# Kernel tuning notes

Measured on AMD Instinct MI355X. Metric: run time of the kernel, lower is better.

Reference implementation:

```python
import jax, jax.numpy as jnp
import numpy as np

N = 100_000      # nodes
E = 1_600_000    # edges (avg degree 16)
F_IN = 128       # in_feats
H = 128          # n_hidden
H2 = 64          # n_hidden // 2


def setup_inputs() -> dict:
    key = jax.random.key(0)
    k1, k2, k3, k4, k5 = jax.random.split(key, 5)
    features = jax.random.normal(k1, (N, F_IN), dtype=jnp.float32)
    W1 = jax.random.normal(k2, (F_IN, H), dtype=jnp.float32) * 0.05
    W2 = jax.random.normal(k3, (H, H2), dtype=jnp.float32) * 0.05
    src = jax.random.randint(k4, (E,), 0, N, dtype=jnp.int32)
    dst = jax.random.randint(k5, (E,), 0, N, dtype=jnp.int32)
    return {"features": features, "W1": W1, "W2": W2, "src": src, "dst": dst}


def _graph_conv(h, W, src, dst, out_norm, in_norm):
    # DGL GraphConv, norm='both', bias=False:
    #   rst = D_dst^{-1/2} * (A @ (D_src^{-1/2} * h)) @ W
    # (weight applied before/after aggregation is mathematically identical)
    h = h * out_norm[:, None]                                   # scale source feats
    agg = jax.ops.segment_sum(h[src], dst, num_segments=N)      # SpMM: sum over in-edges
    return (agg * in_norm[:, None]) @ W


def reference(features, W1, W2, src, dst):
    ones = jnp.ones(src.shape[0], dtype=jnp.float32)
    # allow_zero_in_degree=True -> DGL clamps degrees to min 1 for norm
    out_deg = jnp.clip(jax.ops.segment_sum(ones, src, num_segments=N), 1.0)
    in_deg = jnp.clip(jax.ops.segment_sum(ones, dst, num_segments=N), 1.0)
    out_norm = out_deg ** -0.5
    in_norm = in_deg ** -0.5
    h = _graph_conv(features, W1, src, dst, out_norm, in_norm)  # [N, H]
    h = jax.nn.relu(h)
    return _graph_conv(h, W2, src, dst, out_norm, in_norm)      # [N, H2]
```

## Files before the change

kernel.cpp:

```cpp
#include <hip/hip_runtime.h>
#include <cstdint>
#include <cstddef>

#define NN 100000
#define NE 1600000
#define FD 128
#define HD2 64

#define BSH 7
#define BSZ 128
#define NB ((NN + BSZ - 1) / BSZ)
#define TILE 4096
#define NTILE ((NE + TILE - 1) / TILE)
#define CAPB 2560
#define NPREP ((NN * 32 + FD * 64 + HD2 * 64 + 255) / 256)

static_assert(NB <= 1024, "bucket scan assumes <=1024 buckets");

typedef short bf16x8_t __attribute__((ext_vector_type(8)));
typedef float f32x4_t __attribute__((ext_vector_type(4)));
typedef unsigned char uchar;

static __device__ __forceinline__ uint f2bf(float x) {
  uint u = __float_as_uint(x);
  return (u + 0x7fffu + ((u >> 16) & 1u)) >> 16;
}
static __device__ __forceinline__ uint pack2(float lo, float hi) {
  return f2bf(lo) | (f2bf(hi) << 16);
}
static __device__ __forceinline__ float bflo(uint v) { return __uint_as_float(v << 16); }
static __device__ __forceinline__ float bfhi(uint v) { return __uint_as_float(v & 0xffff0000u); }

static __device__ __forceinline__ float dec_w(uint r) {
  return __uint_as_float(((r >> 17) + 0x38000u) << 12);
}

__global__ void k_bucket_prep(const int* __restrict__ src, const int* __restrict__ dst,
                              int* __restrict__ bcnt_d, int* __restrict__ bcnt_s,
                              uint* __restrict__ brec_d, uchar* __restrict__ brec_s,
                              const float* __restrict__ feat, uint* __restrict__ Xraw,
                              const float* __restrict__ W1, const float* __restrict__ W2,
                              uint* __restrict__ W1t, uint* __restrict__ W2t) {
  __shared__ int h[NB];
  __shared__ int gb[NB];
  __shared__ int ls[NB];
  __shared__ int psum[256];
  __shared__ int ntot;
  __shared__ ushort bkt[TILE];
  __shared__ uint lrec[TILE];
  const int bid = blockIdx.x;
  const int t = threadIdx.x;
  if (bid >= 2 * NTILE) {
    int i = (bid - 2 * NTILE) * 256 + t;
    if (i < NN * 32) {
      float4 f = *(const float4*)(feat + 4 * (size_t)i);
      uint2 o;
      o.x = pack2(f.x, f.y);
      o.y = pack2(f.z, f.w);
      *(uint2*)(Xraw + 2 * (size_t)i) = o;
    } else {
      int j = i - NN * 32;
      if (j < FD * 64) {
        int n = j >> 6, kk = j & 63;
        W1t[j] = pack2(W1[(size_t)(2 * kk) * FD + n], W1[(size_t)(2 * kk + 1) * FD + n]);
      } else if (j < FD * 64 + HD2 * 64) {
        int j2 = j - FD * 64;
        int n = j2 >> 6, kk = j2 & 63;
        W2t[j2] = pack2(W2[(size_t)(2 * kk) * HD2 + n], W2[(size_t)(2 * kk + 1) * HD2 + n]);
      }
    }
    return;
  }
  const bool is_dst = bid < NTILE;
  const int* key = is_dst ? dst : src;
  const int base = (is_dst ? bid : bid - NTILE) * TILE;
  for (int i = t; i < NB; i += 256) h[i] = 0;
  __syncthreads();
  for (int i = t; i < TILE; i += 256) {
    int e = base + i;
    if (e < NE) atomicAdd(&h[key[e] >> BSH], 1);
  }
  __syncthreads();
  int* bcnt = is_dst ? bcnt_d : bcnt_s;
  for (int i = t; i < NB; i += 256) {
    int c = h[i];
    gb[i] = c ? atomicAdd(bcnt + i, c) : 0;
  }
  int i0 = t * 4;
  int c0 = (i0 + 0 < NB) ? h[i0 + 0] : 0;
  int c1 = (i0 + 1 < NB) ? h[i0 + 1] : 0;
  int c2 = (i0 + 2 < NB) ? h[i0 + 2] : 0;
  int c3 = (i0 + 3 < NB) ? h[i0 + 3] : 0;
  int cs = c0 + c1 + c2 + c3;
  psum[t] = cs;
  __syncthreads();
#pragma unroll
  for (int off = 1; off < 256; off <<= 1) {
    int x = (t >= off) ? psum[t - off] : 0;
    __syncthreads();
    psum[t] += x;
    __syncthreads();
  }
  int excl = psum[t] - cs;
  if (i0 + 0 < NB) ls[i0 + 0] = excl;
  if (i0 + 1 < NB) ls[i0 + 1] = excl + c0;
  if (i0 + 2 < NB) ls[i0 + 2] = excl + c0 + c1;
  if (i0 + 3 < NB) ls[i0 + 3] = excl + c0 + c1 + c2;
  if (t == 255) ntot = psum[255];
  __syncthreads();
  for (int i = t; i < NB; i += 256) h[i] = 0;
  __syncthreads();
  if (is_dst) {
    for (int i = t; i < TILE; i += 256) {
      int e = base + i;
      if (e < NE) {
        int d = dst[e], sv = src[e];
        int b = d >> BSH;
        int q = ls[b] + atomicAdd(&h[b], 1);
        lrec[q] = ((uint)(d & (BSZ - 1)) << 17) | (uint)sv;
        bkt[q] = (ushort)b;
      }
    }
  } else {
    for (int i = t; i < TILE; i += 256) {
      int e = base + i;
      if (e < NE) {
        int sv = src[e];
        int b = sv >> BSH;
        int q = ls[b] + atomicAdd(&h[b], 1);
        lrec[q] = (uint)(sv & (BSZ - 1));
        bkt[q] = (ushort)b;
      }
    }
  }
  __syncthreads();
  const int n = ntot;
  if (is_dst) {
    for (int q = t; q < n; q += 256) {
      int b = bkt[q];
      int p = gb[b] + (q - ls[b]);
      if (p < CAPB) brec_d[(size_t)b * CAPB + p] = lrec[q];
    }
  } else {
    for (int q = t; q < n; q += 256) {
      int b = bkt[q];
      int p = gb[b] + (q - ls[b]);
      if (p < CAPB) brec_s[(size_t)b * CAPB + p] = (uchar)lrec[q];
    }
  }
}

__global__ __launch_bounds__(1024) void k_onorm_scan(const uchar* __restrict__ brec_s,
                                                     const int* __restrict__ bcnt_s,
                                                     float* __restrict__ out_norm,
                                                     const int* __restrict__ bcnt_d,
                                                     int* __restrict__ boff_d) {
  __shared__ int sm[1024];
  const int t = threadIdx.x;
  const int b = blockIdx.x;
  if (b < NB) {
    if (t < BSZ) sm[t] = 0;
    __syncthreads();
    const int len = min(bcnt_s[b], CAPB);
    const size_t rbase = (size_t)b * CAPB;
    for (int e = t; e < len; e += 1024)
      atomicAdd(&sm[brec_s[rbase + e]], 1);
    __syncthreads();
    const int s0 = b * BSZ;
    const int ns = min(BSZ, NN - s0);
    if (t < ns) out_norm[s0 + t] = rsqrtf((float)max(sm[t], 1));
  } else {
    int v = (t < NB) ? bcnt_d[t] : 0;
    sm[t] = v;
    __syncthreads();
#pragma unroll
    for (int off = 1; off < 1024; off <<= 1) {
      int x = (t >= off) ? sm[t - off] : 0;
      __syncthreads();
      sm[t] += x;
      __syncthreads();
    }
    if (t < NB) boff_d[t + 1] = sm[t];
    if (t == 0) boff_d[0] = 0;
  }
}

__global__ __launch_bounds__(256) void k_build(const uint* __restrict__ brec_d,
                                               const int* __restrict__ bcnt_d,
                                               const int* __restrict__ boff,
                                               const float* __restrict__ onorm,
                                               int* __restrict__ row_ptr,
                                               float* __restrict__ in_norm,
                                               uint* __restrict__ csr) {
  __shared__ int lcnt[BSZ];
  __shared__ int lscan[BSZ + 1];
  __shared__ int lcur[BSZ];
  __shared__ int lcsr[CAPB];
  const int t = threadIdx.x;
  const int b = blockIdx.x;
  const int d0 = b * BSZ;
  const int nd = min(BSZ, NN - d0);
  const size_t rbase = (size_t)b * CAPB;
  const int len = min(bcnt_d[b], CAPB);
  const int ebase = boff[b];

  for (int i = t; i < BSZ; i += 256) lcnt[i] = 0;
  __syncthreads();
  for (int e = t; e < len; e += 256)
    atomicAdd(&lcnt[brec_d[rbase + e] >> 17], 1);
  __syncthreads();
  for (int i = t; i < nd; i += 256)
    in_norm[d0 + i] = rsqrtf((float)max(lcnt[i], 1));

  if (t < BSZ) lcur[t] = lcnt[t];
  __syncthreads();
#pragma unroll
  for (int off = 1; off < BSZ; off <<= 1) {
    int x = (t >= off && t < BSZ) ? lcur[t - off] : 0;
    __syncthreads();
    if (t < BSZ) lcur[t] += x;
    __syncthreads();
  }
  if (t < BSZ) lscan[t + 1] = lcur[t];
  if (t == 0) lscan[0] = 0;
  __syncthreads();
  for (int i = t; i <= nd; i += 256) row_ptr[d0 + i] = ebase + lscan[i];
  if (t < BSZ) lcur[t] = lscan[t];
  __syncthreads();

  for (int e = t; e < len; e += 256) {
    uint r = brec_d[rbase + e];
    int p = atomicAdd(&lcur[r >> 17], 1);
    lcsr[p] = (int)(r & 0x1FFFFu);
  }
  __syncthreads();
  for (int ld = t; ld < nd; ld += 256) {
    int a = lscan[ld], bnd = lscan[ld + 1];
    for (int i = a + 1; i < bnd; ++i) {
      int v = lcsr[i];
      int j = i - 1;
      while (j >= a && lcsr[j] > v) { lcsr[j + 1] = lcsr[j]; --j; }
      lcsr[j + 1] = v;
    }
  }
  __syncthreads();
  for (int i = t; i < len; i += 256) {
    int s = lcsr[i];
    uint code = (__float_as_uint(onorm[s]) >> 12) - 0x38000u;
    csr[ebase + i] = (code << 17) | (uint)s;
  }
}

__global__ void k_spmm1b(const uint* __restrict__ Xraw, const int* __restrict__ row_ptr,
                         const uint* __restrict__ csr, const float* __restrict__ in_norm,
                         uint* __restrict__ Hb1) {
  int gid = blockIdx.x * blockDim.x + threadIdx.x;
  int row = gid >> 6;
  if (row >= NN) return;
  int lane = threadIdx.x & 63;
  int grp = lane >> 4;
  int gl = lane & 15;
  int e0 = row_ptr[row], e1 = row_ptr[row + 1];
  float2 a0 = {0.f, 0.f}, a1 = {0.f, 0.f}, a2 = {0.f, 0.f}, a3 = {0.f, 0.f};
#define ACCW(v, ww)                                                       \
  a0.x = fmaf(ww, bflo((v).x), a0.x); a0.y = fmaf(ww, bfhi((v).x), a0.y); \
  a1.x = fmaf(ww, bflo((v).y), a1.x); a1.y = fmaf(ww, bfhi((v).y), a1.y); \
  a2.x = fmaf(ww, bflo((v).z), a2.x); a2.y = fmaf(ww, bfhi((v).z), a2.y); \
  a3.x = fmaf(ww, bflo((v).w), a3.x); a3.y = fmaf(ww, bfhi((v).w), a3.y);
  int e = e0;
  for (; e + 16 <= e1; e += 16) {
    uint r0 = csr[e + grp];
    uint r1 = csr[e + 4 + grp];
    uint r2 = csr[e + 8 + grp];
    uint r3 = csr[e + 12 + grp];
    uint4 v0 = *(const uint4*)(Xraw + ((size_t)(r0 & 0x1FFFFu) << 6) + (gl << 2));
    uint4 v1 = *(const uint4*)(Xraw + ((size_t)(r1 & 0x1FFFFu) << 6) + (gl << 2));
    uint4 v2 = *(const uint4*)(Xraw + ((size_t)(r2 & 0x1FFFFu) << 6) + (gl << 2));
    uint4 v3 = *(const uint4*)(Xraw + ((size_t)(r3 & 0x1FFFFu) << 6) + (gl << 2));
    float w0 = dec_w(r0), w1 = dec_w(r1), w2 = dec_w(r2), w3 = dec_w(r3);
    ACCW(v0, w0);
    ACCW(v1, w1);
    ACCW(v2, w2);
    ACCW(v3, w3);
  }
  for (; e + 4 <= e1; e += 4) {
    uint r0 = csr[e + grp];
    uint4 v0 = *(const uint4*)(Xraw + ((size_t)(r0 & 0x1FFFFu) << 6) + (gl << 2));
    float w0 = dec_w(r0);
    ACCW(v0, w0);
  }
  if (e + grp < e1) {
    uint r0 = csr[e + grp];
    uint4 v0 = *(const uint4*)(Xraw + ((size_t)(r0 & 0x1FFFFu) << 6) + (gl << 2));
    float w0 = dec_w(r0);
    ACCW(v0, w0);
  }
#undef ACCW
#pragma unroll
  for (int m = 16; m <= 32; m <<= 1) {
    a0.x += __shfl_xor(a0.x, m); a0.y += __shfl_xor(a0.y, m);
    a1.x += __shfl_xor(a1.x, m); a1.y += __shfl_xor(a1.y, m);
    a2.x += __shfl_xor(a2.x, m); a2.y += __shfl_xor(a2.y, m);
    a3.x += __shfl_xor(a3.x, m); a3.y += __shfl_xor(a3.y, m);
  }
  if (grp == 0) {
    float wi = in_norm[row];
    uint4 o;
    o.x = pack2(a0.x * wi, a0.y * wi);
    o.y = pack2(a1.x * wi, a1.y * wi);
    o.z = pack2(a2.x * wi, a2.y * wi);
    o.w = pack2(a3.x * wi, a3.y * wi);
    *(uint4*)(Hb1 + ((size_t)row << 6) + (gl << 2)) = o;
  }
}

__global__ __launch_bounds__(256) void k_mlp(const uint* __restrict__ Hb1,
                                             const uint* __restrict__ W1t,
                                             const uint* __restrict__ W2t,
                                             const float* __restrict__ onorm,
                                             ushort* __restrict__ Tb) {
  __shared__ ushort h_lds[64 * FD];
  char* const lds = (char*)h_lds;
  const int tid = threadIdx.x;
  const int wid = tid >> 6;
  const int lane = tid & 63;
  const int l15 = lane & 15;
  const int g = lane >> 4;
  const int rowbase = blockIdx.x * 64 + wid * 16;

  const int ar = min(rowbase + l15, NN - 1);
  const uint* Arow = Hb1 + (size_t)ar * 64;
  bf16x8_t afr[4];
#pragma unroll
  for (int kc = 0; kc < 4; ++kc)
    afr[kc] = *(const bf16x8_t*)(Arow + kc * 16 + g * 4);

  float wnorm[4];
#pragma unroll
  for (int r = 0; r < 4; ++r)
    wnorm[r] = onorm[min(rowbase + 4 * g + r, NN - 1)];

#pragma unroll
  for (int nf = 0; nf < 8; ++nf) {
    f32x4_t acc = {0.f, 0.f, 0.f, 0.f};
#pragma unroll
    for (int kc = 0; kc < 4; ++kc) {
      bf16x8_t b = *(const bf16x8_t*)(W1t + (size_t)(nf * 16 + l15) * 64 + kc * 16 + g * 4);
      acc = __builtin_amdgcn_mfma_f32_16x16x32_bf16(afr[kc], b, acc, 0, 0, 0);
    }
#pragma unroll
    for (int r = 0; r < 4; ++r) {
      float hv = fmaxf(acc[r], 0.f) * wnorm[r];
      int row = wid * 16 + 4 * g + r;
      int byte = row * 256 + (nf * 16 + l15) * 2;
      byte ^= (row & 7) << 4;
      *(ushort*)(lds + byte) = (ushort)f2bf(hv);
    }
  }
  __syncthreads();

  bf16x8_t a2[4];
#pragma unroll
  for (int kc = 0; kc < 4; ++kc) {
    int row = wid * 16 + l15;
    int byte = row * 256 + (kc * 32 + 8 * g) * 2;
    byte ^= (row & 7) << 4;
    a2[kc] = *(const bf16x8_t*)(lds + byte);
  }
#pragma unroll
  for (int nf = 0; nf < 4; ++nf) {
    f32x4_t acc = {0.f, 0.f, 0.f, 0.f};
#pragma unroll
    for (int kc = 0; kc < 4; ++kc) {
      bf16x8_t b = *(const bf16x8_t*)(W2t + (size_t)(nf * 16 + l15) * 64 + kc * 16 + g * 4);
      acc = __builtin_amdgcn_mfma_f32_16x16x32_bf16(a2[kc], b, acc, 0, 0, 0);
    }
#pragma unroll
    for (int r = 0; r < 4; ++r) {
      int row = rowbase + 4 * g + r;
      if (row < NN)
        Tb[(size_t)row * HD2 + nf * 16 + l15] = (ushort)f2bf(acc[r]);
    }
  }
}

__global__ void k_spmm2b(const uint* __restrict__ Tb, const int* __restrict__ row_ptr,
                         const uint* __restrict__ csr, const float* __restrict__ in_norm,
                         float* __restrict__ out) {
  int gid = blockIdx.x * blockDim.x + threadIdx.x;
  int row = gid >> 6;
  if (row >= NN) return;
  int lane = threadIdx.x & 63;
  int grp = lane >> 4;
  int gl = lane & 15;
  int e0 = row_ptr[row], e1 = row_ptr[row + 1];
  float2 a0 = {0.f, 0.f}, a1 = {0.f, 0.f};
#define ACC2(v)                                  \
  a0.x += bflo((v).x); a0.y += bfhi((v).x);      \
  a1.x += bflo((v).y); a1.y += bfhi((v).y);
  int e = e0;
  for (; e + 16 <= e1; e += 16) {
    uint s0 = csr[e + grp] & 0x1FFFFu;
    uint s1 = csr[e + 4 + grp] & 0x1FFFFu;
    uint s2 = csr[e + 8 + grp] & 0x1FFFFu;
    uint s3 = csr[e + 12 + grp] & 0x1FFFFu;
    uint2 v0 = *(const uint2*)(Tb + ((size_t)s0 << 5) + (gl << 1));
    uint2 v1 = *(const uint2*)(Tb + ((size_t)s1 << 5) + (gl << 1));
    uint2 v2 = *(const uint2*)(Tb + ((size_t)s2 << 5) + (gl << 1));
    uint2 v3 = *(const uint2*)(Tb + ((size_t)s3 << 5) + (gl << 1));
    ACC2(v0);
    ACC2(v1);
    ACC2(v2);
    ACC2(v3);
  }
  for (; e + 4 <= e1; e += 4) {
    uint s0 = csr[e + grp] & 0x1FFFFu;
    uint2 v0 = *(const uint2*)(Tb + ((size_t)s0 << 5) + (gl << 1));
    ACC2(v0);
  }
  if (e + grp < e1) {
    uint s0 = csr[e + grp] & 0x1FFFFu;
    uint2 v0 = *(const uint2*)(Tb + ((size_t)s0 << 5) + (gl << 1));
    ACC2(v0);
  }
#undef ACC2
#pragma unroll
  for (int m = 16; m <= 32; m <<= 1) {
    a0.x += __shfl_xor(a0.x, m); a0.y += __shfl_xor(a0.y, m);
    a1.x += __shfl_xor(a1.x, m); a1.y += __shfl_xor(a1.y, m);
  }
  if (grp == 0) {
    float wi = in_norm[row];
    *(float4*)(out + (size_t)row * HD2 + gl * 4) =
        make_float4(a0.x * wi, a0.y * wi, a1.x * wi, a1.y * wi);
  }
}

extern "C" void kernel_launch(void* const* d_in, const int* in_sizes, int n_in,
                              void* d_out, int out_size, void* d_ws, size_t ws_size,
                              hipStream_t stream) {
  const float* feat = (const float*)d_in[0];
  const float* W1   = (const float*)d_in[1];
  const float* W2   = (const float*)d_in[2];
  const int*   src  = (const int*)d_in[3];
  const int*   dst  = (const int*)d_in[4];
  float* out = (float*)d_out;

  char* p = (char*)d_ws;
  auto take = [&p](size_t bytes) -> char* {
    char* r = p;
    p += (bytes + 511) & ~(size_t)511;
    return r;
  };
  int*   row_ptr  = (int*)take((size_t)(NN + 1) * 4);
  int*   bcnt     = (int*)take((size_t)2 * NB * 4);
  int*   boff_d   = (int*)take((size_t)(NB + 1) * 4);
  float* out_norm = (float*)take((size_t)NN * 4);
  float* in_norm  = (float*)take((size_t)NN * 4);
  uint*  csr      = (uint*)take((size_t)NE * 4);
  uint*  W1t      = (uint*)take((size_t)FD * 64 * 4);
  uint*  W2t      = (uint*)take((size_t)HD2 * 64 * 4);
  uint*  Xraw     = (uint*)take((size_t)NN * 64 * 4);
  uint*  Hb1      = (uint*)take((size_t)NN * 64 * 4);
  int*   bcnt_d   = bcnt;
  int*   bcnt_s   = bcnt + NB;
  ushort* Tb      = (ushort*)Xraw;
  uint*   brec_d  = (uint*)Hb1;
  uchar*  brec_s  = (uchar*)(Hb1 + (size_t)NB * CAPB);

  hipMemsetAsync(bcnt, 0, (size_t)2 * NB * 4, stream);

  k_bucket_prep<<<2 * NTILE + NPREP, 256, 0, stream>>>(src, dst, bcnt_d, bcnt_s, brec_d, brec_s,
                                                       feat, Xraw, W1, W2, W1t, W2t);
  k_onorm_scan <<<NB + 1, 1024, 0, stream>>>(brec_s, bcnt_s, out_norm, bcnt_d, boff_d);
  k_build      <<<NB, 256, 0, stream>>>(brec_d, bcnt_d, boff_d, out_norm,
                                        row_ptr, in_norm, csr);

  k_spmm1b<<<(NN * 64) / 256, 256, 0, stream>>>(Xraw, row_ptr, csr, in_norm, Hb1);
  k_mlp   <<<(NN + 63) / 64, 256, 0, stream>>>(Hb1, W1t, W2t, out_norm, Tb);
  k_spmm2b<<<(NN * 64) / 256, 256, 0, stream>>>((const uint*)Tb, row_ptr, csr, in_norm, out);
}
```

Before: 256.2 us.

## Split SpMM feature columns across two blocks per row group

```diff
diff --git a/kernel.cpp b/kernel.cpp
--- a/kernel.cpp
+++ b/kernel.cpp
@@ -16,6 +16,7 @@
 #define NPREP ((NN * 32 + FD * 64 + HD2 * 64 + 255) / 256)
 
 static_assert(NB <= 1024, "bucket scan assumes <=1024 buckets");
+static_assert(NN % 16 == 0, "spmm row mapping assumes NN % 16 == 0");
 
 typedef short bf16x8_t __attribute__((ext_vector_type(8)));
 typedef float f32x4_t __attribute__((ext_vector_type(4)));
@@ -254,29 +255,30 @@
 __global__ void k_spmm1b(const uint* __restrict__ Xraw, const int* __restrict__ row_ptr,
                          const uint* __restrict__ csr, const float* __restrict__ in_norm,
                          uint* __restrict__ Hb1) {
-  int gid = blockIdx.x * blockDim.x + threadIdx.x;
-  int row = gid >> 6;
+  const int bid = blockIdx.x;
+  const int g8 = bid >> 3, r8 = bid & 7;
+  const int cg = r8 >> 2;
+  const int row = (g8 * 4 + (r8 & 3)) * 4 + (threadIdx.x >> 6);
   if (row >= NN) return;
-  int lane = threadIdx.x & 63;
-  int grp = lane >> 4;
-  int gl = lane & 15;
+  const int lane = threadIdx.x & 63;
+  const int grp = lane >> 4;
+  const int gl = lane & 15;
+  const uint coff = (uint)(cg * 32 + gl * 2);
   int e0 = row_ptr[row], e1 = row_ptr[row + 1];
-  float2 a0 = {0.f, 0.f}, a1 = {0.f, 0.f}, a2 = {0.f, 0.f}, a3 = {0.f, 0.f};
+  float2 a0 = {0.f, 0.f}, a1 = {0.f, 0.f};
 #define ACCW(v, ww)                                                       \
   a0.x = fmaf(ww, bflo((v).x), a0.x); a0.y = fmaf(ww, bfhi((v).x), a0.y); \
-  a1.x = fmaf(ww, bflo((v).y), a1.x); a1.y = fmaf(ww, bfhi((v).y), a1.y); \
-  a2.x = fmaf(ww, bflo((v).z), a2.x); a2.y = fmaf(ww, bfhi((v).z), a2.y); \
-  a3.x = fmaf(ww, bflo((v).w), a3.x); a3.y = fmaf(ww, bfhi((v).w), a3.y);
+  a1.x = fmaf(ww, bflo((v).y), a1.x); a1.y = fmaf(ww, bfhi((v).y), a1.y);
   int e = e0;
   for (; e + 16 <= e1; e += 16) {
     uint r0 = csr[e + grp];
     uint r1 = csr[e + 4 + grp];
     uint r2 = csr[e + 8 + grp];
     uint r3 = csr[e + 12 + grp];
-    uint4 v0 = *(const uint4*)(Xraw + ((size_t)(r0 & 0x1FFFFu) << 6) + (gl << 2));
-    uint4 v1 = *(const uint4*)(Xraw + ((size_t)(r1 & 0x1FFFFu) << 6) + (gl << 2));
-    uint4 v2 = *(const uint4*)(Xraw + ((size_t)(r2 & 0x1FFFFu) << 6) + (gl << 2));
-    uint4 v3 = *(const uint4*)(Xraw + ((size_t)(r3 & 0x1FFFFu) << 6) + (gl << 2));
+    uint2 v0 = *(const uint2*)(Xraw + ((size_t)(r0 & 0x1FFFFu) << 6) + coff);
+    uint2 v1 = *(const uint2*)(Xraw + ((size_t)(r1 & 0x1FFFFu) << 6) + coff);
+    uint2 v2 = *(const uint2*)(Xraw + ((size_t)(r2 & 0x1FFFFu) << 6) + coff);
+    uint2 v3 = *(const uint2*)(Xraw + ((size_t)(r3 & 0x1FFFFu) << 6) + coff);
     float w0 = dec_w(r0), w1 = dec_w(r1), w2 = dec_w(r2), w3 = dec_w(r3);
     ACCW(v0, w0);
     ACCW(v1, w1);
@@ -285,13 +287,13 @@
   }
   for (; e + 4 <= e1; e += 4) {
     uint r0 = csr[e + grp];
-    uint4 v0 = *(const uint4*)(Xraw + ((size_t)(r0 & 0x1FFFFu) << 6) + (gl << 2));
+    uint2 v0 = *(const uint2*)(Xraw + ((size_t)(r0 & 0x1FFFFu) << 6) + coff);
     float w0 = dec_w(r0);
     ACCW(v0, w0);
   }
   if (e + grp < e1) {
     uint r0 = csr[e + grp];
-    uint4 v0 = *(const uint4*)(Xraw + ((size_t)(r0 & 0x1FFFFu) << 6) + (gl << 2));
+    uint2 v0 = *(const uint2*)(Xraw + ((size_t)(r0 & 0x1FFFFu) << 6) + coff);
     float w0 = dec_w(r0);
     ACCW(v0, w0);
   }
@@ -300,17 +302,13 @@
   for (int m = 16; m <= 32; m <<= 1) {
     a0.x += __shfl_xor(a0.x, m); a0.y += __shfl_xor(a0.y, m);
     a1.x += __shfl_xor(a1.x, m); a1.y += __shfl_xor(a1.y, m);
-    a2.x += __shfl_xor(a2.x, m); a2.y += __shfl_xor(a2.y, m);
-    a3.x += __shfl_xor(a3.x, m); a3.y += __shfl_xor(a3.y, m);
   }
   if (grp == 0) {
     float wi = in_norm[row];
-    uint4 o;
+    uint2 o;
     o.x = pack2(a0.x * wi, a0.y * wi);
     o.y = pack2(a1.x * wi, a1.y * wi);
-    o.z = pack2(a2.x * wi, a2.y * wi);
-    o.w = pack2(a3.x * wi, a3.y * wi);
-    *(uint4*)(Hb1 + ((size_t)row << 6) + (gl << 2)) = o;
+    *(uint2*)(Hb1 + ((size_t)row << 6) + coff) = o;
   }
 }
 
@@ -387,27 +385,28 @@
 __global__ void k_spmm2b(const uint* __restrict__ Tb, const int* __restrict__ row_ptr,
                          const uint* __restrict__ csr, const float* __restrict__ in_norm,
                          float* __restrict__ out) {
-  int gid = blockIdx.x * blockDim.x + threadIdx.x;
-  int row = gid >> 6;
+  const int bid = blockIdx.x;
+  const int g8 = bid >> 3, r8 = bid & 7;
+  const int cg = r8 >> 2;
+  const int row = (g8 * 4 + (r8 & 3)) * 4 + (threadIdx.x >> 6);
   if (row >= NN) return;
-  int lane = threadIdx.x & 63;
-  int grp = lane >> 4;
-  int gl = lane & 15;
+  const int lane = threadIdx.x & 63;
+  const int grp = lane >> 4;
+  const int gl = lane & 15;
+  const uint coff = (uint)(cg * 16 + gl);
   int e0 = row_ptr[row], e1 = row_ptr[row + 1];
-  float2 a0 = {0.f, 0.f}, a1 = {0.f, 0.f};
-#define ACC2(v)                                  \
-  a0.x += bflo((v).x); a0.y += bfhi((v).x);      \
-  a1.x += bflo((v).y); a1.y += bfhi((v).y);
+  float2 a0 = {0.f, 0.f};
+#define ACC2(v)  a0.x += bflo(v); a0.y += bfhi(v);
   int e = e0;
   for (; e + 16 <= e1; e += 16) {
     uint s0 = csr[e + grp] & 0x1FFFFu;
     uint s1 = csr[e + 4 + grp] & 0x1FFFFu;
     uint s2 = csr[e + 8 + grp] & 0x1FFFFu;
     uint s3 = csr[e + 12 + grp] & 0x1FFFFu;
-    uint2 v0 = *(const uint2*)(Tb + ((size_t)s0 << 5) + (gl << 1));
-    uint2 v1 = *(const uint2*)(Tb + ((size_t)s1 << 5) + (gl << 1));
-    uint2 v2 = *(const uint2*)(Tb + ((size_t)s2 << 5) + (gl << 1));
-    uint2 v3 = *(const uint2*)(Tb + ((size_t)s3 << 5) + (gl << 1));
+    uint v0 = Tb[((size_t)s0 << 5) + coff];
+    uint v1 = Tb[((size_t)s1 << 5) + coff];
+    uint v2 = Tb[((size_t)s2 << 5) + coff];
+    uint v3 = Tb[((size_t)s3 << 5) + coff];
     ACC2(v0);
     ACC2(v1);
     ACC2(v2);
@@ -415,24 +414,24 @@
   }
   for (; e + 4 <= e1; e += 4) {
     uint s0 = csr[e + grp] & 0x1FFFFu;
-    uint2 v0 = *(const uint2*)(Tb + ((size_t)s0 << 5) + (gl << 1));
+    uint v0 = Tb[((size_t)s0 << 5) + coff];
     ACC2(v0);
   }
   if (e + grp < e1) {
     uint s0 = csr[e + grp] & 0x1FFFFu;
-    uint2 v0 = *(const uint2*)(Tb + ((size_t)s0 << 5) + (gl << 1));
+    uint v0 = Tb[((size_t)s0 << 5) + coff];
     ACC2(v0);
   }
 #undef ACC2
 #pragma unroll
   for (int m = 16; m <= 32; m <<= 1) {
-    a0.x += __shfl_xor(a0.x, m); a0.y += __shfl_xor(a0.y, m);
-    a1.x += __shfl_xor(a1.x, m); a1.y += __shfl_xor(a1.y, m);
+    a0.x += __shfl_xor(a0.x, m);
+    a0.y += __shfl_xor(a0.y, m);
   }
   if (grp == 0) {
     float wi = in_norm[row];
-    *(float4*)(out + (size_t)row * HD2 + gl * 4) =
-        make_float4(a0.x * wi, a0.y * wi, a1.x * wi, a1.y * wi);
+    *(float2*)(out + (size_t)row * HD2 + cg * 32 + gl * 2) =
+        make_float2(a0.x * wi, a0.y * wi);
   }
 }
 
@@ -476,7 +475,7 @@
   k_build      <<<NB, 256, 0, stream>>>(brec_d, bcnt_d, boff_d, out_norm,
                                         row_ptr, in_norm, csr);
 
-  k_spmm1b<<<(NN * 64) / 256, 256, 0, stream>>>(Xraw, row_ptr, csr, in_norm, Hb1);
+  k_spmm1b<<<2 * (NN / 4), 256, 0, stream>>>(Xraw, row_ptr, csr, in_norm, Hb1);
   k_mlp   <<<(NN + 63) / 64, 256, 0, stream>>>(Hb1, W1t, W2t, out_norm, Tb);
-  k_spmm2b<<<(NN * 64) / 256, 256, 0, stream>>>((const uint*)Tb, row_ptr, csr, in_norm, out);
-}
+  k_spmm2b<<<2 * (NN / 4), 256, 0, stream>>>((const uint*)Tb, row_ptr, csr, in_norm, out);
+}
```

Measured after the change: 323.6 us. +26.3%, slower.

## Fuse first-layer SpMM aggregation with MLP kernel via LDS staging

Applied to the files above, without the earlier changes.

```diff
diff --git a/kernel.cpp b/kernel.cpp
--- a/kernel.cpp
+++ b/kernel.cpp
@@ -251,94 +251,103 @@
   }
 }
 
-__global__ void k_spmm1b(const uint* __restrict__ Xraw, const int* __restrict__ row_ptr,
-                         const uint* __restrict__ csr, const float* __restrict__ in_norm,
-                         uint* __restrict__ Hb1) {
-  int gid = blockIdx.x * blockDim.x + threadIdx.x;
-  int row = gid >> 6;
-  if (row >= NN) return;
-  int lane = threadIdx.x & 63;
-  int grp = lane >> 4;
-  int gl = lane & 15;
-  int e0 = row_ptr[row], e1 = row_ptr[row + 1];
-  float2 a0 = {0.f, 0.f}, a1 = {0.f, 0.f}, a2 = {0.f, 0.f}, a3 = {0.f, 0.f};
+__global__ __launch_bounds__(256) void k_spmm_mlp(const uint* __restrict__ Xraw,
+                                                  const int* __restrict__ row_ptr,
+                                                  const uint* __restrict__ csr,
+                                                  const float* __restrict__ in_norm,
+                                                  const uint* __restrict__ W1t,
+                                                  const uint* __restrict__ W2t,
+                                                  const float* __restrict__ onorm,
+                                                  ushort* __restrict__ Tb) {
+  __shared__ ushort h_lds[64 * FD];
+  char* const lds = (char*)h_lds;
+  const int tid = threadIdx.x;
+  const int wid = tid >> 6;
+  const int lane = tid & 63;
+  const int grp = lane >> 4;
+  const int gl = lane & 15;
+  const int l15 = lane & 15;
+  const int g = lane >> 4;
+  const int rowbase = blockIdx.x * 64;
+
+  for (int i = 0; i < 16; ++i) {
+    const int rl = wid * 16 + i;
+    const int row = rowbase + rl;
+    float2 a0 = {0.f, 0.f}, a1 = {0.f, 0.f}, a2 = {0.f, 0.f}, a3 = {0.f, 0.f};
+    if (row < NN) {
+      int e0 = row_ptr[row], e1 = row_ptr[row + 1];
 #define ACCW(v, ww)                                                       \
   a0.x = fmaf(ww, bflo((v).x), a0.x); a0.y = fmaf(ww, bfhi((v).x), a0.y); \
   a1.x = fmaf(ww, bflo((v).y), a1.x); a1.y = fmaf(ww, bfhi((v).y), a1.y); \
   a2.x = fmaf(ww, bflo((v).z), a2.x); a2.y = fmaf(ww, bfhi((v).z), a2.y); \
   a3.x = fmaf(ww, bflo((v).w), a3.x); a3.y = fmaf(ww, bfhi((v).w), a3.y);
-  int e = e0;
-  for (; e + 16 <= e1; e += 16) {
-    uint r0 = csr[e + grp];
-    uint r1 = csr[e + 4 + grp];
-    uint r2 = csr[e + 8 + grp];
-    uint r3 = csr[e + 12 + grp];
-    uint4 v0 = *(const uint4*)(Xraw + ((size_t)(r0 & 0x1FFFFu) << 6) + (gl << 2));
-    uint4 v1 = *(const uint4*)(Xraw + ((size_t)(r1 & 0x1FFFFu) << 6) + (gl << 2));
-    uint4 v2 = *(const uint4*)(Xraw + ((size_t)(r2 & 0x1FFFFu) << 6) + (gl << 2));
-    uint4 v3 = *(const uint4*)(Xraw + ((size_t)(r3 & 0x1FFFFu) << 6) + (gl << 2));
-    float w0 = dec_w(r0), w1 = dec_w(r1), w2 = dec_w(r2), w3 = dec_w(r3);
-    ACCW(v0, w0);
-    ACCW(v1, w1);
-    ACCW(v2, w2);
-    ACCW(v3, w3);
-  }
-  for (; e + 4 <= e1; e += 4) {
-    uint r0 = csr[e + grp];
-    uint4 v0 = *(const uint4*)(Xraw + ((size_t)(r0 & 0x1FFFFu) << 6) + (gl << 2));
-    float w0 = dec_w(r0);
-    ACCW(v0, w0);
-  }
-  if (e + grp < e1) {
-    uint r0 = csr[e + grp];
-    uint4 v0 = *(const uint4*)(Xraw + ((size_t)(r0 & 0x1FFFFu) << 6) + (gl << 2));
-    float w0 = dec_w(r0);
-    ACCW(v0, w0);
-  }
+      int e = e0;
+      for (; e + 16 <= e1; e += 16) {
+        uint r0 = csr[e + grp];
+        uint r1 = csr[e + 4 + grp];
+        uint r2 = csr[e + 8 + grp];
+        uint r3 = csr[e + 12 + grp];
+        uint4 v0 = *(const uint4*)(Xraw + ((size_t)(r0 & 0x1FFFFu) << 6) + (gl << 2));
+        uint4 v1 = *(const uint4*)(Xraw + ((size_t)(r1 & 0x1FFFFu) << 6) + (gl << 2));
+        uint4 v2 = *(const uint4*)(Xraw + ((size_t)(r2 & 0x1FFFFu) << 6) + (gl << 2));
+        uint4 v3 = *(const uint4*)(Xraw + ((size_t)(r3 & 0x1FFFFu) << 6) + (gl << 2));
+        float w0 = dec_w(r0), w1 = dec_w(r1), w2 = dec_w(r2), w3 = dec_w(r3);
+        ACCW(v0, w0);
+        ACCW(v1, w1);
+        ACCW(v2, w2);
+        ACCW(v3, w3);
+      }
+      for (; e + 4 <= e1; e += 4) {
+        uint r0 = csr[e + grp];
+        uint4 v0 = *(const uint4*)(Xraw + ((size_t)(r0 & 0x1FFFFu) << 6) + (gl << 2));
+        float w0 = dec_w(r0);
+        ACCW(v0, w0);
+      }
+      if (e + grp < e1) {
+        uint r0 = csr[e + grp];
+        uint4 v0 = *(const uint4*)(Xraw + ((size_t)(r0 & 0x1FFFFu) << 6) + (gl << 2));
+        float w0 = dec_w(r0);
+        ACCW(v0, w0);
+      }
 #undef ACCW
 #pragma unroll
-  for (int m = 16; m <= 32; m <<= 1) {
-    a0.x += __shfl_xor(a0.x, m); a0.y += __shfl_xor(a0.y, m);
-    a1.x += __shfl_xor(a1.x, m); a1.y += __shfl_xor(a1.y, m);
-    a2.x += __shfl_xor(a2.x, m); a2.y += __shfl_xor(a2.y, m);
-    a3.x += __shfl_xor(a3.x, m); a3.y += __shfl_xor(a3.y, m);
-  }
-  if (grp == 0) {
-    float wi = in_norm[row];
-    uint4 o;
-    o.x = pack2(a0.x * wi, a0.y * wi);
-    o.y = pack2(a1.x * wi, a1.y * wi);
-    o.z = pack2(a2.x * wi, a2.y * wi);
-    o.w = pack2(a3.x * wi, a3.y * wi);
-    *(uint4*)(Hb1 + ((size_t)row << 6) + (gl << 2)) = o;
-  }
-}
-
-__global__ __launch_bounds__(256) void k_mlp(const uint* __restrict__ Hb1,
-                                             const uint* __restrict__ W1t,
-                                             const uint* __restrict__ W2t,
-                                             const float* __restrict__ onorm,
-                                             ushort* __restrict__ Tb) {
-  __shared__ ushort h_lds[64 * FD];
-  char* const lds = (char*)h_lds;
-  const int tid = threadIdx.x;
-  const int wid = tid >> 6;
-  const int lane = tid & 63;
-  const int l15 = lane & 15;
-  const int g = lane >> 4;
-  const int rowbase = blockIdx.x * 64 + wid * 16;
-
-  const int ar = min(rowbase + l15, NN - 1);
-  const uint* Arow = Hb1 + (size_t)ar * 64;
+      for (int m = 16; m <= 32; m <<= 1) {
+        a0.x += __shfl_xor(a0.x, m); a0.y += __shfl_xor(a0.y, m);
+        a1.x += __shfl_xor(a1.x, m); a1.y += __shfl_xor(a1.y, m);
+        a2.x += __shfl_xor(a2.x, m); a2.y += __shfl_xor(a2.y, m);
+        a3.x += __shfl_xor(a3.x, m); a3.y += __shfl_xor(a3.y, m);
+      }
+    }
+    if (grp == 0) {
+      uint4 o = {0u, 0u, 0u, 0u};
+      if (row < NN) {
+        float wi = in_norm[row];
+        o.x = pack2(a0.x * wi, a0.y * wi);
+        o.y = pack2(a1.x * wi, a1.y * wi);
+        o.z = pack2(a2.x * wi, a2.y * wi);
+        o.w = pack2(a3.x * wi, a3.y * wi);
+      }
+      int byte = rl * 256 + gl * 16;
+      byte ^= (rl & 7) << 4;
+      *(uint4*)(lds + byte) = o;
+    }
+  }
+  __syncthreads();
+
+  const int arl = wid * 16 + l15;
   bf16x8_t afr[4];
 #pragma unroll
-  for (int kc = 0; kc < 4; ++kc)
-    afr[kc] = *(const bf16x8_t*)(Arow + kc * 16 + g * 4);
-
+  for (int kc = 0; kc < 4; ++kc) {
+    int byte = arl * 256 + kc * 64 + g * 16;
+    byte ^= (arl & 7) << 4;
+    afr[kc] = *(const bf16x8_t*)(lds + byte);
+  }
   float wnorm[4];
+  const int wrowbase = rowbase + wid * 16;
 #pragma unroll
   for (int r = 0; r < 4; ++r)
-    wnorm[r] = onorm[min(rowbase + 4 * g + r, NN - 1)];
+    wnorm[r] = onorm[min(wrowbase + 4 * g + r, NN - 1)];
+  __syncthreads();
 
 #pragma unroll
   for (int nf = 0; nf < 8; ++nf) {
@@ -377,7 +386,7 @@
     }
 #pragma unroll
     for (int r = 0; r < 4; ++r) {
-      int row = rowbase + 4 * g + r;
+      int row = wrowbase + 4 * g + r;
       if (row < NN)
         Tb[(size_t)row * HD2 + nf * 16 + l15] = (ushort)f2bf(acc[r]);
     }
@@ -461,12 +470,14 @@
   uint*  W1t      = (uint*)take((size_t)FD * 64 * 4);
   uint*  W2t      = (uint*)take((size_t)HD2 * 64 * 4);
   uint*  Xraw     = (uint*)take((size_t)NN * 64 * 4);
-  uint*  Hb1      = (uint*)take((size_t)NN * 64 * 4);
+  uint*  recbuf   = (uint*)take((size_t)NB * CAPB * 4 + (size_t)NB * CAPB);
   int*   bcnt_d   = bcnt;
   int*   bcnt_s   = bcnt + NB;
   ushort* Tb      = (ushort*)Xraw;
-  uint*   brec_d  = (uint*)Hb1;
-  uchar*  brec_s  = (uchar*)(Hb1 + (size_t)NB * CAPB);
+  ushort* Tb_real = (ushort*)take((size_t)NN * HD2 * 2);
+  uint*   brec_d  = recbuf;
+  uchar*  brec_s  = (uchar*)(recbuf + (size_t)NB * CAPB);
+  (void)Tb;
 
   hipMemsetAsync(bcnt, 0, (size_t)2 * NB * 4, stream);
 
@@ -476,7 +487,8 @@
   k_build      <<<NB, 256, 0, stream>>>(brec_d, bcnt_d, boff_d, out_norm,
                                         row_ptr, in_norm, csr);
 
-  k_spmm1b<<<(NN * 64) / 256, 256, 0, stream>>>(Xraw, row_ptr, csr, in_norm, Hb1);
-  k_mlp   <<<(NN + 63) / 64, 256, 0, stream>>>(Hb1, W1t, W2t, out_norm, Tb);
-  k_spmm2b<<<(NN * 64) / 256, 256, 0, stream>>>((const uint*)Tb, row_ptr, csr, in_norm, out);
-}
+  k_spmm_mlp<<<(NN + 63) / 64, 256, 0, stream>>>(Xraw, row_ptr, csr, in_norm,
+                                                 W1t, W2t, out_norm, Tb_real);
+  k_spmm2b  <<<(NN * 64) / 256, 256, 0, stream>>>((const uint*)Tb_real, row_ptr, csr,
+                                                  in_norm, out);
+}
```

After: 283.9 us. 1.11x slower.
